# Performance work log

Hardware: AMD Instinct MI355X
Metric: run time of the kernel (lower is better)

## Reference

```python
import jax, jax.numpy as jnp
import numpy as np

B, D_IN, D, D_OUT, N_BLOCKS = 32768, 100, 1024, 1, 5
H = 0.1
EPS = 1e-4


def setup_inputs() -> dict:
    key = jax.random.key(0)
    ks = jax.random.split(key, 10)
    x = jax.random.normal(ks[0], (B, D_IN), dtype=jnp.float32)
    # first linear: D_IN -> D
    W0 = jax.random.normal(ks[1], (D, D_IN), dtype=jnp.float32) / np.sqrt(D_IN)
    b0 = jnp.zeros((D,), dtype=jnp.float32)
    # middle residual linears: D -> D, stacked over blocks
    Ws = jax.random.normal(ks[2], (N_BLOCKS, D, D), dtype=jnp.float32) / np.sqrt(D)
    bs = jnp.zeros((N_BLOCKS, D), dtype=jnp.float32)
    # brownian Linear(D, 1, bias=False) weight vectors, one per block
    bw = jax.random.normal(ks[3], (N_BLOCKS, D), dtype=jnp.float32) / np.sqrt(D)
    # last linear: D -> D_OUT
    Wlast = jax.random.normal(ks[4], (D_OUT, D), dtype=jnp.float32) / np.sqrt(D)
    blast = jnp.zeros((D_OUT,), dtype=jnp.float32)
    # torch.rand_like(out): uniform [0,1) noise per block
    noise = jax.random.uniform(ks[5], (N_BLOCKS, B, D), dtype=jnp.float32)
    return {"x": x, "W0": W0, "b0": b0, "Ws": Ws, "bs": bs,
            "bw": bw, "Wlast": Wlast, "blast": blast, "noise": noise}


def reference(x, W0, b0, Ws, bs, bw, Wlast, blast, noise):
    sqrt_h = H ** 0.5
    out = jnp.tanh(x @ W0.T + b0)  # [B, D]
    for i in range(N_BLOCKS):
        z = noise[i]  # [B, D]
        w = bw[i]     # [D]
        # product(): z @ (w w^T + eps I)^T = (z.w) w + eps z  (rank-1, O(D))
        proj = (z @ w)[:, None] * w + EPS * z
        out = out + H * jnp.tanh(out @ Ws[i].T + bs[i]) + sqrt_h * proj
    return out @ Wlast.T + blast  # [B, D_OUT]
```

## Files before the change

kernel.cpp:

```cpp
#include <hip/hip_runtime.h>
#include <hip/hip_bf16.h>


typedef unsigned short u16;
typedef __attribute__((ext_vector_type(8))) short short8;
typedef __attribute__((ext_vector_type(8))) u16 u16x8;
typedef __attribute__((ext_vector_type(4))) u16 u16x4;
typedef __attribute__((ext_vector_type(4))) float f32x4;

#define BROWS 32768
#define DDIM 1024
#define NBLK 5
#define H_STEP 0.1f
#define SQRT_H 0.31622776601683794f

#define FENCE() asm volatile("" ::: "memory")
#define BARRIER() do { FENCE(); __builtin_amdgcn_s_barrier(); FENCE(); } while (0)

__device__ __forceinline__ float bf2f(u16 u) {
    return __uint_as_float(((unsigned)u) << 16);
}
__device__ __forceinline__ u16 f2bf(float f) {
    unsigned u = __float_as_uint(f);
    unsigned r = 0x7fffu + ((u >> 16) & 1u);
    return (u16)((u + r) >> 16);
}
__device__ __forceinline__ float fast_tanh(float s) {
    float e = __expf(2.0f * s);
    return 1.0f - 2.0f * __builtin_amdgcn_rcpf(e + 1.0f);
}

#define GLOAD_LDS16(g, l)                                                        \
    __builtin_amdgcn_global_load_lds(                                            \
        (const __attribute__((address_space(1))) unsigned int*)(const void*)(g), \
        (__attribute__((address_space(3))) unsigned int*)(void*)(l), 16, 0, 0)

__global__ __launch_bounds__(256) void pad_cvt(const float* __restrict__ src,
                                               u16* __restrict__ dst,
                                               int R, int C, int Cp) {
    int idx = blockIdx.x * 256 + threadIdx.x;
    if (idx >= R * Cp) return;
    int r = idx / Cp;
    int c = idx - r * Cp;
    float v = (c < C) ? src[(size_t)r * C + c] : 0.0f;
    dst[idx] = f2bf(v);
}

__global__ __launch_bounds__(256) void zw_kernel(const float* __restrict__ noise,
                                                 const float* __restrict__ bw,
                                                 float* __restrict__ zw) {
    int gw = (blockIdx.x * 256 + threadIdx.x) >> 6;
    int lane = threadIdx.x & 63;
    if (gw >= NBLK * BROWS) return;
    int i = gw >> 15;
    const float* zr = noise + (size_t)gw * DDIM;
    const float* wr = bw + i * DDIM;
    float s = 0.0f;
#pragma unroll
    for (int it = 0; it < 4; ++it) {
        int k = it * 256 + lane * 4;
        f32x4 z = *(const f32x4*)(zr + k);
        f32x4 w = *(const f32x4*)(wr + k);
        s += z.x * w.x + z.y * w.y + z.z * w.z + z.w * w.w;
    }
#pragma unroll
    for (int off = 32; off > 0; off >>= 1) s += __shfl_down(s, off, 64);
    if (lane == 0) zw[gw] = s;
}

template <int KK, int EPI>
__global__ __launch_bounds__(512, 2) void gemm256(const u16* __restrict__ Ag,
                                                  const u16* __restrict__ Bg,
                                                  const float* __restrict__ bias,
                                                  u16* __restrict__ outW,
                                                  const u16* __restrict__ outR,
                                                  const float* __restrict__ zw,
                                                  const float* __restrict__ bwv) {
    constexpr int NT = KK / 64;
    __shared__ __align__(16) u16 smem[65536];
    char* lds = (char*)smem;

    const int bid = blockIdx.x;
    const int swz = (bid & 7) * 64 + (bid >> 3);
    const int row0 = (swz >> 2) * 256;
    const int col0 = (swz & 3) * 256;

    const int tid = threadIdx.x;
    const int lane = tid & 63;
    const int wid = tid >> 6;
    const int wm = wid >> 2;
    const int wn = wid & 3;

    const int srow = tid >> 2;
    const int skq = (tid & 3) ^ ((tid >> 3) & 3);
    const u16* agp0 = Ag + (size_t)(row0 + srow) * KK + skq * 8;
    const u16* agp1 = Ag + (size_t)(row0 + 128 + srow) * KK + skq * 8;
    const u16* bgp0 = Bg + (size_t)(col0 + srow) * KK + skq * 8;
    const u16* bgp1 = Bg + (size_t)(col0 + 128 + srow) * KK + skq * 8;
    char* lp0 = lds + (tid >> 6) * 1024;

    auto stage = [&](int t, int half) {
        if (t >= NT) return;
        const int is_b = half & 1;
        const int kh = half >> 1;
        const int koff = t * 64 + kh * 32;
        char* dst = lp0 + ((t & 1) << 16) + (is_b << 15) + (kh << 14);
        const u16* g0 = (is_b ? bgp0 : agp0) + koff;
        const u16* g1 = (is_b ? bgp1 : agp1) + koff;
        GLOAD_LDS16(g0, dst);
        GLOAD_LDS16(g1, dst + 8192);
    };

    const int g_swz = (lane >> 1) & 3;
    const int rchunk = ((lane >> 4) ^ g_swz) << 4;
    const int aoff = (wm * 128 + (lane & 15)) * 64 + rchunk;
    const int boff = 32768 + (wn * 64 + (lane & 15)) * 64 + rchunk;

    short8 af[8];
    short8 bfr[2];
    f32x4 acc[8][4];
#pragma unroll
    for (int m = 0; m < 8; ++m)
#pragma unroll
        for (int n = 0; n < 4; ++n) acc[m][n] = (f32x4){0.f, 0.f, 0.f, 0.f};

#define LOAD_A(kh, bufc)                                                              \
    do {                                                                              \
        _Pragma("unroll") for (int m = 0; m < 8; ++m)                                 \
            af[m] = *(const short8*)(lds + aoff + m * 1024 + (kh) * 16384 + (bufc) * 65536); \
    } while (0)
#define LOAD_B(kh, hn, bufc)                                                          \
    do {                                                                              \
        bfr[0] = *(const short8*)(lds + boff + ((hn) * 2 + 0) * 1024 + (kh) * 16384 + (bufc) * 65536); \
        bfr[1] = *(const short8*)(lds + boff + ((hn) * 2 + 1) * 1024 + (kh) * 16384 + (bufc) * 65536); \
    } while (0)
#define MFMA16(hn)                                                                    \
    do {                                                                              \
        _Pragma("unroll") for (int m = 0; m < 8; ++m) {                               \
            acc[m][(hn) * 2 + 0] = __builtin_amdgcn_mfma_f32_16x16x32_bf16(af[m], bfr[0], acc[m][(hn) * 2 + 0], 0, 0, 0); \
            acc[m][(hn) * 2 + 1] = __builtin_amdgcn_mfma_f32_16x16x32_bf16(af[m], bfr[1], acc[m][(hn) * 2 + 1], 0, 0, 0); \
        }                                                                             \
    } while (0)
#define PHASE(kh, hn, bufc, STAGE, VMW)                                               \
    do {                                                                              \
        if ((hn) == 0) LOAD_A(kh, bufc);                                              \
        LOAD_B(kh, hn, bufc);                                                         \
        STAGE;                                                                        \
        FENCE(); __builtin_amdgcn_s_barrier();                                        \
        asm volatile("s_waitcnt lgkmcnt(0)" ::: "memory");                            \
        __builtin_amdgcn_s_setprio(1);                                                \
        MFMA16(hn);                                                                   \
        __builtin_amdgcn_s_setprio(0);                                                \
        VMW;                                                                          \
        FENCE(); __builtin_amdgcn_s_barrier(); FENCE();                               \
    } while (0)
#define VMW_TAIL(kt)                                                                  \
    do {                                                                              \
        if ((kt) < NT - 2)      asm volatile("s_waitcnt vmcnt(6)" ::: "memory");      \
        else if ((kt) == NT - 2) asm volatile("s_waitcnt vmcnt(0)" ::: "memory");     \
    } while (0)
#define TILE(kt, bufc)                                                                \
    do {                                                                              \
        PHASE(0, 0, bufc, stage((kt) + 1, 3), ((void)0));                             \
        PHASE(0, 1, bufc, stage((kt) + 2, 0), ((void)0));                             \
        PHASE(1, 0, bufc, stage((kt) + 2, 1), ((void)0));                             \
        PHASE(1, 1, bufc, stage((kt) + 2, 2), VMW_TAIL(kt));                          \
    } while (0)

    stage(0, 0); stage(0, 1); stage(0, 2); stage(0, 3);
    stage(1, 0); stage(1, 1); stage(1, 2);
    asm volatile("s_waitcnt vmcnt(6)" ::: "memory");
    BARRIER();

    for (int kt2 = 0; kt2 < NT / 2; ++kt2) {
        TILE(2 * kt2, 0);
        TILE(2 * kt2 + 1, 1);
    }

    float bcol[4];
#pragma unroll
    for (int ng = 0; ng < 4; ++ng) bcol[ng] = bias[col0 + wn * 64 + ng * 16 + (lane & 15)];

    char* wbase = lds + wid * 16384;
    const int lr0 = (lane >> 4) * 4;
    const int lc0 = lane & 15;
#pragma unroll
    for (int m = 0; m < 8; ++m) {
#pragma unroll
        for (int ng = 0; ng < 4; ++ng) {
#pragma unroll
            for (int j = 0; j < 4; ++j) {
                int lrow = m * 16 + lr0 + j;
                int lcol = ng * 16 + lc0;
                float t = fast_tanh(acc[m][ng][j] + bcol[ng]);
                float d = (EPI == 0) ? t : H_STEP * t;
                int chunk = (lcol >> 3) ^ ((lrow >> 2) & 7);
                *(u16*)(wbase + lrow * 128 + (chunk << 4) + (lcol & 7) * 2) = f2bf(d);
            }
        }
    }

    const int gr_base = row0 + wm * 128;
    const int gc_base = col0 + wn * 64;
#pragma unroll
    for (int it = 0; it < 16; ++it) {
        int lrow = it * 8 + (lane >> 3);
        int chunk = lane & 7;
        int schunk = chunk ^ ((lrow >> 2) & 7);
        u16x8 d8 = *(const u16x8*)(wbase + lrow * 128 + (schunk << 4));
        int grow = gr_base + lrow;
        int gcol = gc_base + chunk * 8;
        size_t gidx = (size_t)grow * DDIM + gcol;
        u16x8 o8;
        if constexpr (EPI == 0) {
            o8 = d8;
        } else {
            u16x8 old8 = *(const u16x8*)(outR + gidx);
            float zr = SQRT_H * zw[grow];
            f32x4 bw0 = *(const f32x4*)(bwv + gcol);
            f32x4 bw1 = *(const f32x4*)(bwv + gcol + 4);
#pragma unroll
            for (int e = 0; e < 8; ++e) {
                float bwe = (e < 4) ? bw0[e] : bw1[e - 4];
                float v = bf2f(old8[e]) + bf2f(d8[e]) + zr * bwe;
                o8[e] = f2bf(v);
            }
        }
        *(u16x8*)(outW + gidx) = o8;
    }
#undef LOAD_A
#undef LOAD_B
#undef MFMA16
#undef PHASE
#undef VMW_TAIL
#undef TILE
}

__global__ __launch_bounds__(256) void last_k(const u16* __restrict__ out,
                                              const float* __restrict__ wlast,
                                              const float* __restrict__ blast,
                                              float* __restrict__ y) {
    int gw = (blockIdx.x * 256 + threadIdx.x) >> 6;
    int lane = threadIdx.x & 63;
    if (gw >= BROWS) return;
    const u16* orow = out + (size_t)gw * DDIM;
    float s = 0.0f;
#pragma unroll
    for (int it = 0; it < 4; ++it) {
        int k = it * 256 + lane * 4;
        u16x4 o = *(const u16x4*)(orow + k);
        f32x4 w = *(const f32x4*)(wlast + k);
        s += bf2f(o.x) * w.x + bf2f(o.y) * w.y + bf2f(o.z) * w.z + bf2f(o.w) * w.w;
    }
#pragma unroll
    for (int off = 32; off > 0; off >>= 1) s += __shfl_down(s, off, 64);
    if (lane == 0) y[gw] = s + blast[0];
}

extern "C" void kernel_launch(void* const* d_in, const int* in_sizes, int n_in,
                              void* d_out, int out_size, void* d_ws, size_t ws_size,
                              hipStream_t stream) {
    const float* x     = (const float*)d_in[0];
    const float* W0    = (const float*)d_in[1];
    const float* b0    = (const float*)d_in[2];
    const float* Ws    = (const float*)d_in[3];
    const float* bs    = (const float*)d_in[4];
    const float* bw    = (const float*)d_in[5];
    const float* Wlast = (const float*)d_in[6];
    const float* blast = (const float*)d_in[7];
    const float* noise = (const float*)d_in[8];
    float* y = (float*)d_out;
    (void)in_sizes; (void)n_in; (void)out_size; (void)ws_size;

    char* ws = (char*)d_ws;
    size_t off = 0;
    auto alloc = [&](size_t bytes) {
        char* p = ws + off;
        off += (bytes + 255) & ~(size_t)255;
        return p;
    };
    u16* outB0 = (u16*)alloc((size_t)BROWS * DDIM * 2);
    u16* outB1 = (u16*)alloc((size_t)BROWS * DDIM * 2);
    u16* xb    = (u16*)alloc((size_t)BROWS * 128 * 2);
    u16* W0b   = (u16*)alloc((size_t)DDIM * 128 * 2);
    u16* Wsb   = (u16*)alloc((size_t)NBLK * DDIM * DDIM * 2);
    float* zw  = (float*)alloc((size_t)NBLK * BROWS * 4);

    pad_cvt<<<(BROWS * 128 + 255) / 256, 256, 0, stream>>>(x, xb, BROWS, 100, 128);
    pad_cvt<<<(DDIM * 128 + 255) / 256, 256, 0, stream>>>(W0, W0b, DDIM, 100, 128);
    pad_cvt<<<(NBLK * DDIM * DDIM + 255) / 256, 256, 0, stream>>>(Ws, Wsb, NBLK * DDIM, DDIM, DDIM);

    zw_kernel<<<(NBLK * BROWS) / 4, 256, 0, stream>>>(noise, bw, zw);

    gemm256<128, 0><<<512, 512, 0, stream>>>(xb, W0b, b0, outB0,
                                             nullptr, nullptr, nullptr);

    u16* cur = outB0;
    u16* nxt = outB1;
    for (int i = 0; i < NBLK; ++i) {
        gemm256<1024, 1><<<512, 512, 0, stream>>>(
            cur, Wsb + (size_t)i * DDIM * DDIM, bs + (size_t)i * DDIM, nxt, cur,
            zw + (size_t)i * BROWS, bw + (size_t)i * DDIM);
        u16* t = cur; cur = nxt; nxt = t;
    }

    last_k<<<BROWS / 4, 256, 0, stream>>>(cur, Wlast, blast, y);
}
```

Baseline: 591.0 us.

## Double-buffer LDS fragment registers to overlap ds_reads with MFMA in GEMM

Restructures the GEMM main loop so A and B fragments are loaded from LDS into alternate register sets (P/Q) one phase ahead of the MFMAs that consume them. This removes the lgkmcnt(0) wait before each MFMA burst. The final k-tiles are peeled into an explicit epilogue without staging guards, and the vmcnt wait thresholds are retuned. It doubles fragment register usage, which risks spills or lower occupancy under the 512-thread, 2-block launch bounds. It also relies on implicit LDS-read ordering across barriers now that the explicit lgkmcnt wait is gone.

```diff
diff --git a/kernel.cpp b/kernel.cpp
--- a/kernel.cpp
+++ b/kernel.cpp
@@ -77,6 +77,7 @@
                                                   const float* __restrict__ zw,
                                                   const float* __restrict__ bwv) {
     constexpr int NT = KK / 64;
+    static_assert(NT >= 2 && (NT & 1) == 0, "NT even, >=2");
     __shared__ __align__(16) u16 smem[65536];
     char* lds = (char*)smem;
 
@@ -97,10 +98,9 @@
     const u16* agp1 = Ag + (size_t)(row0 + 128 + srow) * KK + skq * 8;
     const u16* bgp0 = Bg + (size_t)(col0 + srow) * KK + skq * 8;
     const u16* bgp1 = Bg + (size_t)(col0 + 128 + srow) * KK + skq * 8;
-    char* lp0 = lds + (tid >> 6) * 1024;
+    char* lp0 = lds + wid * 1024;
 
     auto stage = [&](int t, int half) {
-        if (t >= NT) return;
         const int is_b = half & 1;
         const int kh = half >> 1;
         const int koff = t * 64 + kh * 32;
@@ -111,71 +111,80 @@
         GLOAD_LDS16(g1, dst + 8192);
     };
 
-    const int g_swz = (lane >> 1) & 3;
-    const int rchunk = ((lane >> 4) ^ g_swz) << 4;
+    const int rchunk = ((lane >> 4) ^ ((lane >> 1) & 3)) << 4;
     const int aoff = (wm * 128 + (lane & 15)) * 64 + rchunk;
     const int boff = 32768 + (wn * 64 + (lane & 15)) * 64 + rchunk;
 
-    short8 af[8];
-    short8 bfr[2];
+    short8 afP[8], afQ[8], bfP[2], bfQ[2];
     f32x4 acc[8][4];
 #pragma unroll
     for (int m = 0; m < 8; ++m)
 #pragma unroll
         for (int n = 0; n < 4; ++n) acc[m][n] = (f32x4){0.f, 0.f, 0.f, 0.f};
 
-#define LOAD_A(kh, bufc)                                                              \
+#define PF_A(dst, kh, bufc)                                                           \
     do {                                                                              \
         _Pragma("unroll") for (int m = 0; m < 8; ++m)                                 \
-            af[m] = *(const short8*)(lds + aoff + m * 1024 + (kh) * 16384 + (bufc) * 65536); \
-    } while (0)
-#define LOAD_B(kh, hn, bufc)                                                          \
-    do {                                                                              \
-        bfr[0] = *(const short8*)(lds + boff + ((hn) * 2 + 0) * 1024 + (kh) * 16384 + (bufc) * 65536); \
-        bfr[1] = *(const short8*)(lds + boff + ((hn) * 2 + 1) * 1024 + (kh) * 16384 + (bufc) * 65536); \
-    } while (0)
-#define MFMA16(hn)                                                                    \
+            dst[m] = *(const short8*)(lds + aoff + m * 1024 + (kh) * 16384 + (bufc) * 65536); \
+    } while (0)
+#define PF_B(dst, kh, hn, bufc)                                                       \
+    do {                                                                              \
+        dst[0] = *(const short8*)(lds + boff + ((hn) * 2 + 0) * 1024 + (kh) * 16384 + (bufc) * 65536); \
+        dst[1] = *(const short8*)(lds + boff + ((hn) * 2 + 1) * 1024 + (kh) * 16384 + (bufc) * 65536); \
+    } while (0)
+#define MFMA16(af, bf, hn)                                                            \
     do {                                                                              \
         _Pragma("unroll") for (int m = 0; m < 8; ++m) {                               \
-            acc[m][(hn) * 2 + 0] = __builtin_amdgcn_mfma_f32_16x16x32_bf16(af[m], bfr[0], acc[m][(hn) * 2 + 0], 0, 0, 0); \
-            acc[m][(hn) * 2 + 1] = __builtin_amdgcn_mfma_f32_16x16x32_bf16(af[m], bfr[1], acc[m][(hn) * 2 + 1], 0, 0, 0); \
+            acc[m][(hn) * 2 + 0] = __builtin_amdgcn_mfma_f32_16x16x32_bf16(af[m], bf[0], acc[m][(hn) * 2 + 0], 0, 0, 0); \
+            acc[m][(hn) * 2 + 1] = __builtin_amdgcn_mfma_f32_16x16x32_bf16(af[m], bf[1], acc[m][(hn) * 2 + 1], 0, 0, 0); \
         }                                                                             \
     } while (0)
-#define PHASE(kh, hn, bufc, STAGE, VMW)                                               \
-    do {                                                                              \
-        if ((hn) == 0) LOAD_A(kh, bufc);                                              \
-        LOAD_B(kh, hn, bufc);                                                         \
-        STAGE;                                                                        \
-        FENCE(); __builtin_amdgcn_s_barrier();                                        \
-        asm volatile("s_waitcnt lgkmcnt(0)" ::: "memory");                            \
+#define PHASE(STG, af, bf, hn, VMW, ...)                                              \
+    do {                                                                              \
+        __VA_ARGS__;                                                                  \
+        STG;                                                                          \
+        FENCE(); __builtin_amdgcn_s_barrier(); FENCE();                               \
         __builtin_amdgcn_s_setprio(1);                                                \
-        MFMA16(hn);                                                                   \
+        MFMA16(af, bf, hn);                                                           \
         __builtin_amdgcn_s_setprio(0);                                                \
         VMW;                                                                          \
         FENCE(); __builtin_amdgcn_s_barrier(); FENCE();                               \
     } while (0)
-#define VMW_TAIL(kt)                                                                  \
-    do {                                                                              \
-        if ((kt) < NT - 2)      asm volatile("s_waitcnt vmcnt(6)" ::: "memory");      \
-        else if ((kt) == NT - 2) asm volatile("s_waitcnt vmcnt(0)" ::: "memory");     \
-    } while (0)
-#define TILE(kt, bufc)                                                                \
-    do {                                                                              \
-        PHASE(0, 0, bufc, stage((kt) + 1, 3), ((void)0));                             \
-        PHASE(0, 1, bufc, stage((kt) + 2, 0), ((void)0));                             \
-        PHASE(1, 0, bufc, stage((kt) + 2, 1), ((void)0));                             \
-        PHASE(1, 1, bufc, stage((kt) + 2, 2), VMW_TAIL(kt));                          \
+#define VM8 asm volatile("s_waitcnt vmcnt(8)" ::: "memory")
+#define VM4 asm volatile("s_waitcnt vmcnt(4)" ::: "memory")
+#define VM0 asm volatile("s_waitcnt vmcnt(0)" ::: "memory")
+#define NOSTG ((void)0)
+#define NOVM ((void)0)
+#define NOPREF ((void)0)
+
+#define TILE_FULL(kt, c)                                                              \
+    do {                                                                              \
+        PHASE(stage((kt) + 1, 3), afP, bfP, 0, VM8, PF_B(bfQ, 0, 1, c));              \
+        PHASE(stage((kt) + 2, 0), afP, bfQ, 1, NOVM, PF_A(afQ, 1, c); PF_B(bfP, 1, 0, c)); \
+        PHASE(stage((kt) + 2, 1), afQ, bfP, 0, VM8, PF_B(bfQ, 1, 1, c));              \
+        PHASE(stage((kt) + 2, 2), afQ, bfQ, 1, NOVM, PF_A(afP, 0, (c) ^ 1); PF_B(bfP, 0, 0, (c) ^ 1)); \
     } while (0)
 
     stage(0, 0); stage(0, 1); stage(0, 2); stage(0, 3);
     stage(1, 0); stage(1, 1); stage(1, 2);
-    asm volatile("s_waitcnt vmcnt(6)" ::: "memory");
+    asm volatile("s_waitcnt vmcnt(10)" ::: "memory");
     BARRIER();
-
-    for (int kt2 = 0; kt2 < NT / 2; ++kt2) {
-        TILE(2 * kt2, 0);
-        TILE(2 * kt2 + 1, 1);
-    }
+    PF_A(afP, 0, 0);
+    PF_B(bfP, 0, 0, 0);
+
+    for (int kt2 = 0; kt2 < NT / 2 - 1; ++kt2) {
+        const int kt = 2 * kt2;
+        TILE_FULL(kt, 0);
+        TILE_FULL(kt + 1, 1);
+    }
+    PHASE(stage(NT - 1, 3), afP, bfP, 0, VM8, PF_B(bfQ, 0, 1, 0));
+    PHASE(NOSTG, afP, bfQ, 1, NOVM, PF_A(afQ, 1, 0); PF_B(bfP, 1, 0, 0));
+    PHASE(NOSTG, afQ, bfP, 0, VM4, PF_B(bfQ, 1, 1, 0));
+    PHASE(NOSTG, afQ, bfQ, 1, NOVM, PF_A(afP, 0, 1); PF_B(bfP, 0, 0, 1));
+    PHASE(NOSTG, afP, bfP, 0, VM0, PF_B(bfQ, 0, 1, 1));
+    PHASE(NOSTG, afP, bfQ, 1, NOVM, PF_A(afQ, 1, 1); PF_B(bfP, 1, 0, 1));
+    PHASE(NOSTG, afQ, bfP, 0, NOVM, PF_B(bfQ, 1, 1, 1));
+    PHASE(NOSTG, afQ, bfQ, 1, NOVM, NOPREF);
 
     float bcol[4];
 #pragma unroll
@@ -228,12 +237,17 @@
         }
         *(u16x8*)(outW + gidx) = o8;
     }
-#undef LOAD_A
-#undef LOAD_B
+#undef PF_A
+#undef PF_B
 #undef MFMA16
 #undef PHASE
-#undef VMW_TAIL
-#undef TILE
+#undef VM8
+#undef VM4
+#undef VM0
+#undef NOSTG
+#undef NOVM
+#undef NOPREF
+#undef TILE_FULL
 }
 
 __global__ __launch_bounds__(256) void last_k(const u16* __restrict__ out,
```

Result: slower. 891.6 us (+50.8%).
